# Optimization experiments

Hardware: AMD Instinct MI355X
Metric: run time of the kernel (lower is better)

Reference implementation:

```python
import jax, jax.numpy as jnp
import numpy as np

N_NODES = 100000
N_EDGES = 1600000
IN_DIM = 128
HIDDEN = 128
EPS = 1e-5  # BatchNorm1d default eps


def gcn_conv(x, src, dst, W, b, n_nodes):
    """PyG GCNConv with default add_self_loops=True, edge_weight=None.
    out = D^{-1/2} (A + I) D^{-1/2} X W + b, deg computed from dst (col)."""
    xw = x @ W  # [N, out_dim] -- transform before propagate, as in PyG
    ones = jnp.ones((src.shape[0],), dtype=x.dtype)
    deg = jax.ops.segment_sum(ones, dst, num_segments=n_nodes) + 1.0  # +1 self-loop
    dis = jax.lax.rsqrt(deg)  # deg >= 1 always
    norm = dis[src] * dis[dst]  # [E]
    msgs = xw[src] * norm[:, None]  # [E, out_dim] gather (irregular access)
    agg = jax.ops.segment_sum(msgs, dst, num_segments=n_nodes)
    agg = agg + xw * (1.0 / deg)[:, None]  # self-loop contribution, norm = 1/deg_i
    return agg + b


def batch_norm(x, gamma, beta):
    # training-mode BatchNorm1d: biased batch statistics over the node dim
    m = jnp.mean(x, axis=0)
    v = jnp.mean(jnp.square(x - m), axis=0)
    return gamma * (x - m) * jax.lax.rsqrt(v + EPS) + beta


def setup_inputs() -> dict:
    key = jax.random.key(0)
    ks = jax.random.split(key, 6)
    x = jax.random.normal(ks[0], (N_NODES, IN_DIM), dtype=jnp.float32)
    edge_index = jax.random.randint(ks[1], (2, N_EDGES), 0, N_NODES, dtype=jnp.int64)
    # Glorot-ish scaled weights
    W1 = jax.random.normal(ks[2], (IN_DIM, HIDDEN), dtype=jnp.float32) / np.sqrt(IN_DIM)
    W2 = jax.random.normal(ks[3], (HIDDEN, HIDDEN // 2), dtype=jnp.float32) / np.sqrt(HIDDEN)
    Wf = jax.random.normal(ks[4], (HIDDEN // 2, 1), dtype=jnp.float32) / np.sqrt(HIDDEN // 2)
    return {
        "x": x,
        "edge_index": edge_index,
        "W1": W1, "b1": jnp.zeros((HIDDEN,), jnp.float32),
        "g1": jnp.ones((HIDDEN,), jnp.float32), "beta1": jnp.zeros((HIDDEN,), jnp.float32),
        "W2": W2, "b2": jnp.zeros((HIDDEN // 2,), jnp.float32),
        "g2": jnp.ones((HIDDEN // 2,), jnp.float32), "beta2": jnp.zeros((HIDDEN // 2,), jnp.float32),
        "Wf": Wf, "bf": jnp.zeros((1,), jnp.float32),
    }


def reference(x, edge_index, W1, b1, g1, beta1, W2, b2, g2, beta2, Wf, bf):
    src, dst = edge_index[0], edge_index[1]
    n = x.shape[0]
    h = jax.nn.relu(batch_norm(gcn_conv(x, src, dst, W1, b1, n), g1, beta1))
    # dropout is identity in eval / correctness-baseline mode
    h = jax.nn.relu(batch_norm(gcn_conv(h, src, dst, W2, b2, n), g2, beta2))
    return h @ Wf + bf  # [N, 1]
```

## Files before the change

### kernel.cpp

```cpp
#include <hip/hip_runtime.h>

#define NN 100000
#define NE 1600000
#define D1 128
#define D2 64
#define BN_EPS 1e-5f
#define SCAN_CHUNK 512
#define NB_SCAN ((NN + SCAN_CHUNK - 1) / SCAN_CHUNK)
#define NB_FILL (NE / 512)
#define NB_G1   ((NN + 63) / 64)

typedef unsigned int uint32;
typedef unsigned short ushort;
typedef __attribute__((ext_vector_type(8))) short bf16x8;
typedef __attribute__((ext_vector_type(4))) float f32x4;

__device__ __forceinline__ ushort f2bf1(float f) {
    uint32 u = __float_as_uint(f);
    return (ushort)((u + 0x7FFFu + ((u >> 16) & 1u)) >> 16);
}
__device__ __forceinline__ uint32 f2bf_pair(float a, float b) {
    uint32 ua = __float_as_uint(a), ub = __float_as_uint(b);
    ua = (ua + 0x7FFFu + ((ua >> 16) & 1u)) >> 16;
    ub = (ub + 0x7FFFu + ((ub >> 16) & 1u)) >> 16;
    return ua | (ub << 16);
}
__device__ __forceinline__ float bf_lo(uint32 v) { return __uint_as_float(v << 16); }
__device__ __forceinline__ float bf_hi(uint32 v) { return __uint_as_float(v & 0xFFFF0000u); }

__global__ __launch_bounds__(256) void cnt_k(const int* __restrict__ dst,
                                             int* __restrict__ cnt) {
    int i = blockIdx.x * 256 + threadIdx.x;
    int2 dd = *(const int2*)&dst[2 * i];
    atomicAdd(&cnt[dd.x], 1);
    atomicAdd(&cnt[dd.y], 1);
}

__global__ __launch_bounds__(SCAN_CHUNK) void scan1_k(const int* __restrict__ cnt,
                                                      int* __restrict__ rowptr,
                                                      int* __restrict__ bsum,
                                                      float* __restrict__ dis) {
    __shared__ int sh[SCAN_CHUNK];
    int tid = threadIdx.x;
    int g = blockIdx.x * SCAN_CHUNK + tid;
    int v = (g < NN) ? cnt[g] : 0;
    if (g < NN) dis[g] = rsqrtf((float)v + 1.0f);
    sh[tid] = v;
    __syncthreads();
    for (int o = 1; o < SCAN_CHUNK; o <<= 1) {
        int t = (tid >= o) ? sh[tid - o] : 0;
        __syncthreads();
        sh[tid] += t;
        __syncthreads();
    }
    if (g < NN) rowptr[g] = sh[tid] - v;
    if (tid == SCAN_CHUNK - 1) bsum[blockIdx.x] = sh[tid];
}

__global__ __launch_bounds__(256) void scan23_k(int* __restrict__ rowptr,
                                                const int* __restrict__ bsum) {
    __shared__ int bs[256];
    int tid = threadIdx.x;
    bs[tid] = (tid < NB_SCAN) ? bsum[tid] : 0;
    __syncthreads();
    for (int o = 1; o < 256; o <<= 1) {
        int t = (tid >= o) ? bs[tid - o] : 0;
        __syncthreads();
        bs[tid] += t;
        __syncthreads();
    }
    int g = blockIdx.x * 256 + tid;
    if (g < NN) {
        int chunk = g >> 9;
        int add = (chunk == 0) ? 0 : bs[chunk - 1];
        rowptr[g] += add;
    }
    if (g == 0) rowptr[NN] = NE;
}

__global__ __launch_bounds__(256) void fillgemm_k(const int* __restrict__ src,
                                                  const int* __restrict__ dst,
                                                  const int* __restrict__ rowptr,
                                                  const float* __restrict__ dis,
                                                  int* __restrict__ cur,
                                                  int* __restrict__ esrc,
                                                  float* __restrict__ ew,
                                                  const float* __restrict__ X,
                                                  const ushort* __restrict__ Wt,
                                                  ushort* __restrict__ Yb) {
    if (blockIdx.x < NB_FILL) {
        int i = blockIdx.x * 256 + threadIdx.x;
        int2 ss = *(const int2*)&src[2 * i];
        int2 dd = *(const int2*)&dst[2 * i];
        int p0 = rowptr[dd.x] + atomicAdd(&cur[dd.x], 1);
        esrc[p0] = ss.x;
        ew[p0] = dis[ss.x] * dis[dd.x];
        int p1 = rowptr[dd.y] + atomicAdd(&cur[dd.y], 1);
        esrc[p1] = ss.y;
        ew[p1] = dis[ss.y] * dis[dd.y];
        return;
    }
    const int bid = blockIdx.x - NB_FILL;
    const int lane = threadIdx.x & 63;
    const int wv = threadIdx.x >> 6;
    const int row0 = bid * 64 + wv * 16;
    const int m = lane & 15;
    const int kg = lane >> 4;
    const int rowA = min(row0 + m, NN - 1);
    f32x4 acc[8];
    #pragma unroll
    for (int t = 0; t < 8; ++t) acc[t] = (f32x4){0.f, 0.f, 0.f, 0.f};

    #pragma unroll
    for (int kc = 0; kc < 128; kc += 32) {
        const int k0 = kc + kg * 8;
        float4 xa = *(const float4*)(X + (size_t)rowA * 128 + k0);
        float4 xb = *(const float4*)(X + (size_t)rowA * 128 + k0 + 4);
        bf16x8 af;
        af[0] = (short)f2bf1(xa.x); af[1] = (short)f2bf1(xa.y);
        af[2] = (short)f2bf1(xa.z); af[3] = (short)f2bf1(xa.w);
        af[4] = (short)f2bf1(xb.x); af[5] = (short)f2bf1(xb.y);
        af[6] = (short)f2bf1(xb.z); af[7] = (short)f2bf1(xb.w);
        #pragma unroll
        for (int t = 0; t < 8; ++t) {
            bf16x8 bfr = *(const bf16x8*)(Wt + (size_t)(t * 16 + m) * 128 + k0);
            acc[t] = __builtin_amdgcn_mfma_f32_16x16x32_bf16(af, bfr, acc[t], 0, 0, 0);
        }
    }
    #pragma unroll
    for (int t = 0; t < 8; ++t)
        #pragma unroll
        for (int r = 0; r < 4; ++r) {
            int rr = row0 + kg * 4 + r;
            if (rr < NN) Yb[(size_t)rr * 128 + t * 16 + m] = f2bf1(acc[t][r]);
        }
}

__global__ __launch_bounds__(256) void wt_k(const float* __restrict__ W1,
                                            const float* __restrict__ W2,
                                            ushort* __restrict__ wt1,
                                            ushort* __restrict__ wt2) {
    int i = blockIdx.x * 256 + threadIdx.x;
    if (i < 128 * 128) {
        int c = i >> 7, k = i & 127;
        wt1[i] = f2bf1(W1[k * 128 + c]);
    } else if (i < 128 * 128 + 64 * 128) {
        int o = i - 128 * 128;
        int c = o >> 7, k = o & 127;
        wt2[o] = f2bf1(W2[k * 64 + c]);
    }
}

__global__ __launch_bounds__(256) void mgemm2_k(const ushort* __restrict__ Xb,
                                                const ushort* __restrict__ Wt,
                                                const float* __restrict__ sums,
                                                const float* __restrict__ ssq,
                                                const float* __restrict__ g,
                                                const float* __restrict__ beta,
                                                ushort* __restrict__ Yb) {
    __shared__ float sc[128], shf[128];
    {
        int t = threadIdx.x;
        if (t < 128) {
            float m = sums[t] * (1.0f / NN);
            float var = ssq[t] * (1.0f / NN) - m * m;
            float s = g[t] * rsqrtf(var + BN_EPS);
            sc[t] = s;
            shf[t] = beta[t] - m * s;
        }
    }
    __syncthreads();
    const int lane = threadIdx.x & 63;
    const int wv = threadIdx.x >> 6;
    const int row0 = blockIdx.x * 64 + wv * 16;
    const int m = lane & 15;
    const int kg = lane >> 4;
    const int rowA = min(row0 + m, NN - 1);
    f32x4 acc[4];
    #pragma unroll
    for (int t = 0; t < 4; ++t) acc[t] = (f32x4){0.f, 0.f, 0.f, 0.f};

    #pragma unroll
    for (int kc = 0; kc < 128; kc += 32) {
        const int k0 = kc + kg * 8;
        uint4 raw = *(const uint4*)(Xb + (size_t)rowA * 128 + k0);
        float xs[8];
        xs[0] = bf_lo(raw.x); xs[1] = bf_hi(raw.x);
        xs[2] = bf_lo(raw.y); xs[3] = bf_hi(raw.y);
        xs[4] = bf_lo(raw.z); xs[5] = bf_hi(raw.z);
        xs[6] = bf_lo(raw.w); xs[7] = bf_hi(raw.w);
        float4 sa = *(const float4*)&sc[k0];
        float4 sb = *(const float4*)&sc[k0 + 4];
        float4 ha = *(const float4*)&shf[k0];
        float4 hb = *(const float4*)&shf[k0 + 4];
        xs[0] = fmaxf(fmaf(xs[0], sa.x, ha.x), 0.f);
        xs[1] = fmaxf(fmaf(xs[1], sa.y, ha.y), 0.f);
        xs[2] = fmaxf(fmaf(xs[2], sa.z, ha.z), 0.f);
        xs[3] = fmaxf(fmaf(xs[3], sa.w, ha.w), 0.f);
        xs[4] = fmaxf(fmaf(xs[4], sb.x, hb.x), 0.f);
        xs[5] = fmaxf(fmaf(xs[5], sb.y, hb.y), 0.f);
        xs[6] = fmaxf(fmaf(xs[6], sb.z, hb.z), 0.f);
        xs[7] = fmaxf(fmaf(xs[7], sb.w, hb.w), 0.f);
        bf16x8 af;
        #pragma unroll
        for (int i = 0; i < 8; ++i) af[i] = (short)f2bf1(xs[i]);
        #pragma unroll
        for (int t = 0; t < 4; ++t) {
            bf16x8 bfr = *(const bf16x8*)(Wt + (size_t)(t * 16 + m) * 128 + k0);
            acc[t] = __builtin_amdgcn_mfma_f32_16x16x32_bf16(af, bfr, acc[t], 0, 0, 0);
        }
    }
    #pragma unroll
    for (int t = 0; t < 4; ++t)
        #pragma unroll
        for (int r = 0; r < 4; ++r) {
            int rr = row0 + kg * 4 + r;
            if (rr < NN) Yb[(size_t)rr * 64 + t * 16 + m] = f2bf1(acc[t][r]);
        }
}

__global__ __launch_bounds__(256) void agg128_k(const int* __restrict__ rowptr,
                                                const int* __restrict__ esrc,
                                                const float* __restrict__ ew,
                                                const float* __restrict__ dis,
                                                const uint32* __restrict__ xwb,
                                                const float* __restrict__ b,
                                                uint32* __restrict__ agg1b,
                                                float* __restrict__ sums,
                                                float* __restrict__ ssq) {
    const int lane = threadIdx.x & 63;
    const int wid = (blockIdx.x * 256 + threadIdx.x) >> 6;
    const int nwaves = gridDim.x * 4;
    float s0 = 0.f, s1 = 0.f, q0 = 0.f, q1 = 0.f;
    const float bc0 = b[lane * 2], bc1 = b[lane * 2 + 1];

    for (int n = wid; n < NN; n += nwaves) {
        const int beg = rowptr[n], end = rowptr[n + 1];
        const float dn = dis[n];
        float ax = 0.f, ay = 0.f;
        int e = beg;
        for (; e + 8 <= end; e += 8) {
            int idx[8]; float w[8]; uint32 vv[8];
            #pragma unroll
            for (int j = 0; j < 8; ++j) idx[j] = esrc[e + j];
            #pragma unroll
            for (int j = 0; j < 8; ++j) w[j] = ew[e + j];
            #pragma unroll
            for (int j = 0; j < 8; ++j)
                vv[j] = xwb[(size_t)idx[j] * 64 + lane];
            #pragma unroll
            for (int j = 0; j < 8; ++j) {
                ax = fmaf(bf_lo(vv[j]), w[j], ax);
                ay = fmaf(bf_hi(vv[j]), w[j], ay);
            }
        }
        for (; e < end; ++e) {
            int s = esrc[e];
            float w = ew[e];
            uint32 v = xwb[(size_t)s * 64 + lane];
            ax = fmaf(bf_lo(v), w, ax);
            ay = fmaf(bf_hi(v), w, ay);
        }
        float sl = dn * dn;
        uint32 xv = xwb[(size_t)n * 64 + lane];
        ax = fmaf(bf_lo(xv), sl, ax) + bc0;
        ay = fmaf(bf_hi(xv), sl, ay) + bc1;
        agg1b[(size_t)n * 64 + lane] = f2bf_pair(ax, ay);
        s0 += ax; q0 = fmaf(ax, ax, q0);
        s1 += ay; q1 = fmaf(ay, ay, q1);
    }

    __shared__ float ls[256];
    ls[threadIdx.x] = 0.f;
    __syncthreads();
    atomicAdd(&ls[lane * 2], s0);
    atomicAdd(&ls[lane * 2 + 1], s1);
    atomicAdd(&ls[128 + lane * 2], q0);
    atomicAdd(&ls[128 + lane * 2 + 1], q1);
    __syncthreads();
    if (threadIdx.x < 128) atomicAdd(&sums[threadIdx.x], ls[threadIdx.x]);
    else atomicAdd(&ssq[threadIdx.x - 128], ls[threadIdx.x]);
}

__global__ __launch_bounds__(256) void agg64_k(const int* __restrict__ rowptr,
                                               const int* __restrict__ esrc,
                                               const float* __restrict__ ew,
                                               const float* __restrict__ dis,
                                               const uint32* __restrict__ xwb,
                                               const float* __restrict__ b,
                                               uint32* __restrict__ agg2b,
                                               float* __restrict__ sums,
                                               float* __restrict__ ssq) {
    const int lane = threadIdx.x & 63;
    const int half = lane >> 5;
    const int sl = lane & 31;
    const int wid = (blockIdx.x * 256 + threadIdx.x) >> 6;
    const int nwaves = gridDim.x * 4;
    float s0 = 0.f, s1 = 0.f, q0 = 0.f, q1 = 0.f;
    const float bc0 = b[sl * 2], bc1 = b[sl * 2 + 1];

    for (int n = wid; n < NN; n += nwaves) {
        const int beg = rowptr[n], end = rowptr[n + 1];
        const float dn = dis[n];
        float ax = 0.f, ay = 0.f;
        int e = beg;
        for (; e + 16 <= end; e += 16) {
            int idx[8]; float w[8]; uint32 vv[8];
            #pragma unroll
            for (int j = 0; j < 8; ++j) idx[j] = esrc[e + 2 * j + half];
            #pragma unroll
            for (int j = 0; j < 8; ++j) w[j] = ew[e + 2 * j + half];
            #pragma unroll
            for (int j = 0; j < 8; ++j)
                vv[j] = xwb[(size_t)idx[j] * 32 + sl];
            #pragma unroll
            for (int j = 0; j < 8; ++j) {
                ax = fmaf(bf_lo(vv[j]), w[j], ax);
                ay = fmaf(bf_hi(vv[j]), w[j], ay);
            }
        }
        for (; e + 2 <= end; e += 2) {
            int s = esrc[e + half];
            float w = ew[e + half];
            uint32 v = xwb[(size_t)s * 32 + sl];
            ax = fmaf(bf_lo(v), w, ax);
            ay = fmaf(bf_hi(v), w, ay);
        }
        if (e < end && half == 0) {
            int s = esrc[e];
            float w = ew[e];
            uint32 v = xwb[(size_t)s * 32 + sl];
            ax = fmaf(bf_lo(v), w, ax);
            ay = fmaf(bf_hi(v), w, ay);
        }
        ax += __shfl_down(ax, 32);
        ay += __shfl_down(ay, 32);
        if (half == 0) {
            float slf = dn * dn;
            uint32 xv = xwb[(size_t)n * 32 + sl];
            ax = fmaf(bf_lo(xv), slf, ax) + bc0;
            ay = fmaf(bf_hi(xv), slf, ay) + bc1;
            agg2b[(size_t)n * 32 + sl] = f2bf_pair(ax, ay);
            s0 += ax; q0 = fmaf(ax, ax, q0);
            s1 += ay; q1 = fmaf(ay, ay, q1);
        }
    }

    __shared__ float ls[128];
    if (threadIdx.x < 128) ls[threadIdx.x] = 0.f;
    __syncthreads();
    if (half == 0) {
        atomicAdd(&ls[sl * 2], s0);
        atomicAdd(&ls[sl * 2 + 1], s1);
        atomicAdd(&ls[64 + sl * 2], q0);
        atomicAdd(&ls[64 + sl * 2 + 1], q1);
    }
    __syncthreads();
    if (threadIdx.x < 64) atomicAdd(&sums[threadIdx.x], ls[threadIdx.x]);
    else if (threadIdx.x < 128) atomicAdd(&ssq[threadIdx.x - 64], ls[threadIdx.x]);
}

__global__ __launch_bounds__(256) void final_k(const uint32* __restrict__ h2b,
                                               const float* __restrict__ sums,
                                               const float* __restrict__ ssq,
                                               const float* __restrict__ g,
                                               const float* __restrict__ beta,
                                               const float* __restrict__ Wf,
                                               const float* __restrict__ bf,
                                               float* __restrict__ out) {
    __shared__ float sc[64], shf[64];
    {
        int t = threadIdx.x;
        if (t < 64) {
            float m = sums[t] * (1.0f / NN);
            float var = ssq[t] * (1.0f / NN) - m * m;
            float s = g[t] * rsqrtf(var + BN_EPS);
            sc[t] = s;
            shf[t] = beta[t] - m * s;
        }
    }
    __syncthreads();
    const int lane = threadIdx.x & 63;
    const int half = lane >> 5;
    const int sl = lane & 31;
    const int node = ((blockIdx.x * 256 + threadIdx.x) >> 6) * 2 + half;
    if (node >= NN) return;
    uint32 p = h2b[(size_t)node * 32 + sl];
    float2 wf = *(const float2*)&Wf[sl * 2];
    float v = fmaxf(fmaf(bf_lo(p), sc[sl * 2], shf[sl * 2]), 0.f) * wf.x;
    v = fmaf(fmaxf(fmaf(bf_hi(p), sc[sl * 2 + 1], shf[sl * 2 + 1]), 0.f), wf.y, v);
    #pragma unroll
    for (int o = 16; o > 0; o >>= 1) v += __shfl_down(v, o, 32);
    if (sl == 0) out[node] = v + bf[0];
}

extern "C" void kernel_launch(void* const* d_in, const int* in_sizes, int n_in,
                              void* d_out, int out_size, void* d_ws, size_t ws_size,
                              hipStream_t stream) {
    const float* x   = (const float*)d_in[0];
    const int*   ei  = (const int*)d_in[1];
    const int*   src = ei;
    const int*   dst = ei + NE;
    const float* W1  = (const float*)d_in[2];
    const float* b1  = (const float*)d_in[3];
    const float* g1  = (const float*)d_in[4];
    const float* be1 = (const float*)d_in[5];
    const float* W2  = (const float*)d_in[6];
    const float* b2  = (const float*)d_in[7];
    const float* g2  = (const float*)d_in[8];
    const float* be2 = (const float*)d_in[9];
    const float* Wf  = (const float*)d_in[10];
    const float* bf  = (const float*)d_in[11];
    float* out = (float*)d_out;

    uint32* xwb   = (uint32*)d_ws;
    uint32* agg1b = xwb + (size_t)NN * 64;
    uint32* agg2b = agg1b + (size_t)NN * 64;
    float*  dis   = (float*)(agg2b + (size_t)NN * 32);
    ushort* wt1   = (ushort*)(dis + NN);
    ushort* wt2   = wt1 + 128 * 128;
    int*    rowptr = (int*)(wt2 + 64 * 128);
    int*    bsum   = rowptr + NN + 1;
    int*    esrc   = bsum + 256;
    float*  ew     = (float*)(esrc + NE);
    int*    cnt    = (int*)(ew + NE);
    int*    cur    = cnt + NN;
    float*  sums1  = (float*)(cur + NN);
    float*  ssq1   = sums1 + D1;
    float*  sums2  = ssq1 + D1;
    float*  ssq2   = sums2 + D2;

    hipMemsetAsync(cnt, 0, sizeof(int) * (2 * NN + 2 * D1 + 2 * D2), stream);

    wt_k<<<(128 * 128 + 64 * 128 + 255) / 256, 256, 0, stream>>>(W1, W2, wt1, wt2);
    cnt_k<<<NE / 512, 256, 0, stream>>>(dst, cnt);
    scan1_k<<<NB_SCAN, SCAN_CHUNK, 0, stream>>>(cnt, rowptr, bsum, dis);
    scan23_k<<<(NN + 255) / 256, 256, 0, stream>>>(rowptr, bsum);

    fillgemm_k<<<NB_FILL + NB_G1, 256, 0, stream>>>(src, dst, rowptr, dis, cur, esrc, ew,
                                                    x, wt1, (ushort*)xwb);

    agg128_k<<<2048, 256, 0, stream>>>(rowptr, esrc, ew, dis, xwb, b1, agg1b, sums1, ssq1);

    mgemm2_k<<<(NN + 63) / 64, 256, 0, stream>>>((const ushort*)agg1b, wt2, sums1, ssq1,
                                                 g1, be1, (ushort*)xwb);
    agg64_k<<<2048, 256, 0, stream>>>(rowptr, esrc, ew, dis, xwb, b2, agg2b, sums2, ssq2);

    final_k<<<(NN / 2 + 3) / 4, 256, 0, stream>>>(agg2b, sums2, ssq2, g2, be2, Wf, bf, out);
}
```

Measured before the change: 466.3 us.

## Drop precomputed edge weight array; recompute norm from dis in aggregation; merge wt/cnt kernels

Removes the per-edge weight array ew (written in the CSR fill, read twice in aggregation) and instead computes dis[src]*dis[dst] inside both aggregation kernels from the already gathered source index. This removes the scattered ew writes in fill and the ew stream reads, at the cost of an extra random gather into the 400KB dis array per edge (likely cache-resident). The weight-transpose kernel is also merged into the degree-count kernel, saving one launch.

```diff
diff --git a/kernel.cpp b/kernel.cpp
--- a/kernel.cpp
+++ b/kernel.cpp
@@ -7,6 +7,7 @@
 #define BN_EPS 1e-5f
 #define SCAN_CHUNK 512
 #define NB_SCAN ((NN + SCAN_CHUNK - 1) / SCAN_CHUNK)
+#define NB_WT   ((128 * 128 + 64 * 128 + 255) / 256)
 #define NB_FILL (NE / 512)
 #define NB_G1   ((NN + 63) / 64)
 
@@ -28,9 +29,25 @@
 __device__ __forceinline__ float bf_lo(uint32 v) { return __uint_as_float(v << 16); }
 __device__ __forceinline__ float bf_hi(uint32 v) { return __uint_as_float(v & 0xFFFF0000u); }
 
-__global__ __launch_bounds__(256) void cnt_k(const int* __restrict__ dst,
-                                             int* __restrict__ cnt) {
-    int i = blockIdx.x * 256 + threadIdx.x;
+__global__ __launch_bounds__(256) void wtcnt_k(const float* __restrict__ W1,
+                                               const float* __restrict__ W2,
+                                               ushort* __restrict__ wt1,
+                                               ushort* __restrict__ wt2,
+                                               const int* __restrict__ dst,
+                                               int* __restrict__ cnt) {
+    if (blockIdx.x < NB_WT) {
+        int i = blockIdx.x * 256 + threadIdx.x;
+        if (i < 128 * 128) {
+            int c = i >> 7, k = i & 127;
+            wt1[i] = f2bf1(W1[k * 128 + c]);
+        } else if (i < 128 * 128 + 64 * 128) {
+            int o = i - 128 * 128;
+            int c = o >> 7, k = o & 127;
+            wt2[o] = f2bf1(W2[k * 64 + c]);
+        }
+        return;
+    }
+    int i = (blockIdx.x - NB_WT) * 256 + threadIdx.x;
     int2 dd = *(const int2*)&dst[2 * i];
     atomicAdd(&cnt[dd.x], 1);
     atomicAdd(&cnt[dd.y], 1);
@@ -81,10 +98,8 @@
 __global__ __launch_bounds__(256) void fillgemm_k(const int* __restrict__ src,
                                                   const int* __restrict__ dst,
                                                   const int* __restrict__ rowptr,
-                                                  const float* __restrict__ dis,
                                                   int* __restrict__ cur,
                                                   int* __restrict__ esrc,
-                                                  float* __restrict__ ew,
                                                   const float* __restrict__ X,
                                                   const ushort* __restrict__ Wt,
                                                   ushort* __restrict__ Yb) {
@@ -94,10 +109,8 @@
         int2 dd = *(const int2*)&dst[2 * i];
         int p0 = rowptr[dd.x] + atomicAdd(&cur[dd.x], 1);
         esrc[p0] = ss.x;
-        ew[p0] = dis[ss.x] * dis[dd.x];
         int p1 = rowptr[dd.y] + atomicAdd(&cur[dd.y], 1);
         esrc[p1] = ss.y;
-        ew[p1] = dis[ss.y] * dis[dd.y];
         return;
     }
     const int bid = blockIdx.x - NB_FILL;
@@ -134,21 +147,6 @@
             int rr = row0 + kg * 4 + r;
             if (rr < NN) Yb[(size_t)rr * 128 + t * 16 + m] = f2bf1(acc[t][r]);
         }
-}
-
-__global__ __launch_bounds__(256) void wt_k(const float* __restrict__ W1,
-                                            const float* __restrict__ W2,
-                                            ushort* __restrict__ wt1,
-                                            ushort* __restrict__ wt2) {
-    int i = blockIdx.x * 256 + threadIdx.x;
-    if (i < 128 * 128) {
-        int c = i >> 7, k = i & 127;
-        wt1[i] = f2bf1(W1[k * 128 + c]);
-    } else if (i < 128 * 128 + 64 * 128) {
-        int o = i - 128 * 128;
-        int c = o >> 7, k = o & 127;
-        wt2[o] = f2bf1(W2[k * 64 + c]);
-    }
 }
 
 __global__ __launch_bounds__(256) void mgemm2_k(const ushort* __restrict__ Xb,
@@ -221,7 +219,6 @@
 
 __global__ __launch_bounds__(256) void agg128_k(const int* __restrict__ rowptr,
                                                 const int* __restrict__ esrc,
-                                                const float* __restrict__ ew,
                                                 const float* __restrict__ dis,
                                                 const uint32* __restrict__ xwb,
                                                 const float* __restrict__ b,
@@ -240,14 +237,14 @@
         float ax = 0.f, ay = 0.f;
         int e = beg;
         for (; e + 8 <= end; e += 8) {
-            int idx[8]; float w[8]; uint32 vv[8];
+            int idx[8]; uint32 vv[8]; float w[8];
             #pragma unroll
             for (int j = 0; j < 8; ++j) idx[j] = esrc[e + j];
-            #pragma unroll
-            for (int j = 0; j < 8; ++j) w[j] = ew[e + j];
             #pragma unroll
             for (int j = 0; j < 8; ++j)
                 vv[j] = xwb[(size_t)idx[j] * 64 + lane];
+            #pragma unroll
+            for (int j = 0; j < 8; ++j) w[j] = dis[idx[j]] * dn;
             #pragma unroll
             for (int j = 0; j < 8; ++j) {
                 ax = fmaf(bf_lo(vv[j]), w[j], ax);
@@ -256,7 +253,7 @@
         }
         for (; e < end; ++e) {
             int s = esrc[e];
-            float w = ew[e];
+            float w = dis[s] * dn;
             uint32 v = xwb[(size_t)s * 64 + lane];
             ax = fmaf(bf_lo(v), w, ax);
             ay = fmaf(bf_hi(v), w, ay);
@@ -284,7 +281,6 @@
 
 __global__ __launch_bounds__(256) void agg64_k(const int* __restrict__ rowptr,
                                                const int* __restrict__ esrc,
-                                               const float* __restrict__ ew,
                                                const float* __restrict__ dis,
                                                const uint32* __restrict__ xwb,
                                                const float* __restrict__ b,
@@ -305,14 +301,14 @@
         float ax = 0.f, ay = 0.f;
         int e = beg;
         for (; e + 16 <= end; e += 16) {
-            int idx[8]; float w[8]; uint32 vv[8];
+            int idx[8]; uint32 vv[8]; float w[8];
             #pragma unroll
             for (int j = 0; j < 8; ++j) idx[j] = esrc[e + 2 * j + half];
-            #pragma unroll
-            for (int j = 0; j < 8; ++j) w[j] = ew[e + 2 * j + half];
             #pragma unroll
             for (int j = 0; j < 8; ++j)
                 vv[j] = xwb[(size_t)idx[j] * 32 + sl];
+            #pragma unroll
+            for (int j = 0; j < 8; ++j) w[j] = dis[idx[j]] * dn;
             #pragma unroll
             for (int j = 0; j < 8; ++j) {
                 ax = fmaf(bf_lo(vv[j]), w[j], ax);
@@ -321,14 +317,14 @@
         }
         for (; e + 2 <= end; e += 2) {
             int s = esrc[e + half];
-            float w = ew[e + half];
+            float w = dis[s] * dn;
             uint32 v = xwb[(size_t)s * 32 + sl];
             ax = fmaf(bf_lo(v), w, ax);
             ay = fmaf(bf_hi(v), w, ay);
         }
         if (e < end && half == 0) {
             int s = esrc[e];
-            float w = ew[e];
+            float w = dis[s] * dn;
             uint32 v = xwb[(size_t)s * 32 + sl];
             ax = fmaf(bf_lo(v), w, ax);
             ay = fmaf(bf_hi(v), w, ay);
@@ -422,8 +418,7 @@
     int*    rowptr = (int*)(wt2 + 64 * 128);
     int*    bsum   = rowptr + NN + 1;
     int*    esrc   = bsum + 256;
-    float*  ew     = (float*)(esrc + NE);
-    int*    cnt    = (int*)(ew + NE);
+    int*    cnt    = esrc + NE;
     int*    cur    = cnt + NN;
     float*  sums1  = (float*)(cur + NN);
     float*  ssq1   = sums1 + D1;
@@ -432,19 +427,18 @@
 
     hipMemsetAsync(cnt, 0, sizeof(int) * (2 * NN + 2 * D1 + 2 * D2), stream);
 
-    wt_k<<<(128 * 128 + 64 * 128 + 255) / 256, 256, 0, stream>>>(W1, W2, wt1, wt2);
-    cnt_k<<<NE / 512, 256, 0, stream>>>(dst, cnt);
+    wtcnt_k<<<NB_WT + NE / 512, 256, 0, stream>>>(W1, W2, wt1, wt2, dst, cnt);
     scan1_k<<<NB_SCAN, SCAN_CHUNK, 0, stream>>>(cnt, rowptr, bsum, dis);
     scan23_k<<<(NN + 255) / 256, 256, 0, stream>>>(rowptr, bsum);
 
-    fillgemm_k<<<NB_FILL + NB_G1, 256, 0, stream>>>(src, dst, rowptr, dis, cur, esrc, ew,
+    fillgemm_k<<<NB_FILL + NB_G1, 256, 0, stream>>>(src, dst, rowptr, cur, esrc,
                                                     x, wt1, (ushort*)xwb);
 
-    agg128_k<<<2048, 256, 0, stream>>>(rowptr, esrc, ew, dis, xwb, b1, agg1b, sums1, ssq1);
+    agg128_k<<<2048, 256, 0, stream>>>(rowptr, esrc, dis, xwb, b1, agg1b, sums1, ssq1);
 
     mgemm2_k<<<(NN + 63) / 64, 256, 0, stream>>>((const ushort*)agg1b, wt2, sums1, ssq1,
                                                  g1, be1, (ushort*)xwb);
-    agg64_k<<<2048, 256, 0, stream>>>(rowptr, esrc, ew, dis, xwb, b2, agg2b, sums2, ssq2);
+    agg64_k<<<2048, 256, 0, stream>>>(rowptr, esrc, dis, xwb, b2, agg2b, sums2, ssq2);
 
     final_k<<<(NN / 2 + 3) / 4, 256, 0, stream>>>(agg2b, sums2, ssq2, g2, be2, Wf, bf, out);
 }
```

New measurement: 521.6 us. +11.9%, slower.
